# Optimization experiments

Hardware: AMD Instinct MI355X
Metric: run time of the kernel (lower is better)

The kernel has to match this reference:

```python
import jax, jax.numpy as jnp
import numpy as np

NUM_CLASSES = 512  # P distinct identities in the batch (labels are in [0, P))
TAU = 0.5
EPS = 1e-12


def _l2norm(x):
    # F.normalize(x, dim=1) with eps clamp
    n = jnp.sqrt(jnp.sum(x * x, axis=1, keepdims=True))
    return x / jnp.maximum(n, EPS)


def setup_inputs() -> dict:
    key = jax.random.key(0)
    k1, k2, k3 = jax.random.split(key, 3)
    N, D, P = 8192, 2048, NUM_CLASSES
    feat_vp = jax.random.normal(k1, (N, D), dtype=jnp.float32)
    feat_ap = jax.random.normal(k2, (N, D), dtype=jnp.float32)
    feat_rp = jax.random.normal(k3, (N, D), dtype=jnp.float32)
    # P identities, K = N/P instances each; every class present
    label = (jnp.arange(N) % P).astype(jnp.int32)
    return {"feat_vp": feat_vp, "feat_ap": feat_ap, "feat_rp": feat_rp, "label": label}


def reference(feat_vp, feat_ap, feat_rp, label):
    P = NUM_CLASSES
    fv = _l2norm(feat_vp)
    fa = _l2norm(feat_ap)
    fr = _l2norm(feat_rp)

    # segment-mean over labels (replaces the O(N^2 D) python loop)
    counts = jax.ops.segment_sum(jnp.ones_like(label, dtype=fv.dtype), label,
                                 num_segments=P)  # [P]
    inv_cnt = 1.0 / counts[:, None]

    def centers(f):
        s = jax.ops.segment_sum(f, label, num_segments=P)  # [P, D]
        return _l2norm(s * inv_cnt)

    cv, ca, cr = centers(fv), centers(fa), centers(fr)

    # per-sample centers = unique centers gathered back by label
    loss_intra = (jnp.sum((fv - cv[label]) ** 2, axis=1).mean()
                  + jnp.sum((fa - ca[label]) ** 2, axis=1).mean()
                  + jnp.sum((fr - cr[label]) ** 2, axis=1).mean())

    def pair_loss(c1, c2):
        logits = (c1 @ c2.T) / TAU  # [P, P]
        logp = jax.nn.log_softmax(logits, axis=1)
        return -jnp.mean(jnp.diagonal(logp))

    loss_inter = pair_loss(cv, ca) + pair_loss(cv, cr) + pair_loss(ca, cr)
    return loss_intra + loss_inter
```

## Files before the change

### kernel.cpp

```cpp
#include <hip/hip_runtime.h>
#include <hip/hip_bf16.h>

#define P_CLS 512
#define D_DIM 2048
#define CAP   32
#define TAU_INV 2.0f

typedef short short8 __attribute__((ext_vector_type(8)));
typedef float f32x4 __attribute__((ext_vector_type(4)));

__device__ __forceinline__ unsigned short f2bf_bits(float x) {
  __hip_bfloat16 b = __float2bfloat16(x);
  unsigned short u;
  __builtin_memcpy(&u, &b, sizeof(u));
  return u;
}

__device__ __forceinline__ float xred_sum(float v) {
#pragma unroll
  for (int o = 1; o < 64; o <<= 1) v += __shfl_xor(v, o, 64);
  return v;
}
__device__ __forceinline__ float xred_max(float v) {
#pragma unroll
  for (int o = 1; o < 64; o <<= 1) v = fmaxf(v, __shfl_xor(v, o, 64));
  return v;
}

__global__ void k_init(int* cnt, float* accs) {
  int t = blockIdx.x * blockDim.x + threadIdx.x;
  if (t < P_CLS) cnt[t] = 0;
  if (t < 8) accs[t] = 0.f;
}

__global__ void k_index(const int* __restrict__ label, int* __restrict__ cnt,
                        int* __restrict__ idx, int n) {
  int i = blockIdx.x * blockDim.x + threadIdx.x;
  if (i < n) {
    int p = label[i];
    int slot = atomicAdd(&cnt[p], 1);
    if (slot < CAP) idx[p * CAP + slot] = i;
  }
}

__global__ __launch_bounds__(256)
void k_centers(const float* __restrict__ f0, const float* __restrict__ f1,
               const float* __restrict__ f2, const int* __restrict__ cnt,
               const int* __restrict__ idx, __hip_bfloat16* __restrict__ cb,
               float* __restrict__ accs) {
  __shared__ __align__(16) f32x4 red[4][D_DIM / 4];
  __shared__ float scr[4];
  int p = blockIdx.x, m = blockIdx.y;
  const float* F = (m == 0) ? f0 : (m == 1) ? f1 : f2;
  int t = threadIdx.x, lane = t & 63, wv = t >> 6;
  int c = cnt[p];
  if (c > CAP) c = CAP;
  const int* idxp = idx + p * CAP;

  int nr = (c > wv) ? ((c - wv + 3) >> 2) : 0;

  const f32x4* rp[8];
#pragma unroll
  for (int k = 0; k < 8; ++k) {
    int r = wv + 4 * k;
    int rc = (r < c) ? r : 0;
    rp[k] = (c > 0) ? (const f32x4*)(F + (long)idxp[rc] * D_DIM) + lane
                    : (const f32x4*)F + lane;
  }

  f32x4 acc[8] = {{0,0,0,0},{0,0,0,0},{0,0,0,0},{0,0,0,0},
                  {0,0,0,0},{0,0,0,0},{0,0,0,0},{0,0,0,0}};
  f32x4 ba[8], bb[8], bd[8];

  auto loadrow = [&](f32x4* buf, const f32x4* src) {
#pragma unroll
    for (int j = 0; j < 8; ++j) buf[j] = src[64 * j];
    asm volatile("" : "+v"(buf[0]), "+v"(buf[1]), "+v"(buf[2]), "+v"(buf[3]),
                      "+v"(buf[4]), "+v"(buf[5]), "+v"(buf[6]), "+v"(buf[7]));
  };
  auto consume = [&](const f32x4* buf) {
    float ssq = 0.f;
#pragma unroll
    for (int j = 0; j < 8; ++j) {
      f32x4 q = buf[j] * buf[j];
      ssq += q.x + q.y + q.z + q.w;
    }
    ssq = xred_sum(ssq);
    float w = 1.0f / fmaxf(sqrtf(ssq), 1e-12f);
#pragma unroll
    for (int j = 0; j < 8; ++j) acc[j] += buf[j] * w;
  };

  if (nr > 0) loadrow(ba, rp[0]);
  if (nr > 1) loadrow(bb, rp[1]);
  if (nr > 2) loadrow(bd, rp[2]);
#pragma unroll
  for (int k = 0; k < 8; ++k) {
    f32x4* cur = (k % 3 == 0) ? ba : (k % 3 == 1) ? bb : bd;
    if (k < nr) consume(cur);
    if (k + 3 < nr) loadrow(cur, rp[k + 3]);
  }

#pragma unroll
  for (int j = 0; j < 8; ++j) red[wv][lane + 64 * j] = acc[j];
  __syncthreads();
  f32x4 s0 = red[0][t] + red[1][t] + red[2][t] + red[3][t];
  f32x4 s1 = red[0][t + 256] + red[1][t + 256] + red[2][t + 256] + red[3][t + 256];
  f32x4 q0 = s0 * s0, q1 = s1 * s1;
  float s2 = q0.x + q0.y + q0.z + q0.w + q1.x + q1.y + q1.z + q1.w;
  s2 = xred_sum(s2);
  if (lane == 0) scr[wv] = s2;
  __syncthreads();
  s2 = scr[0] + scr[1] + scr[2] + scr[3];
  float sn = sqrtf(s2);
  float inv = 1.0f / fmaxf(sn, 1e-12f);
  __hip_bfloat16* dst = cb + ((long)m * P_CLS + p) * D_DIM;
  f32x4 o0 = s0 * inv, o1 = s1 * inv;
  ushort4 h0, h1;
  h0.x = f2bf_bits(o0.x); h0.y = f2bf_bits(o0.y);
  h0.z = f2bf_bits(o0.z); h0.w = f2bf_bits(o0.w);
  h1.x = f2bf_bits(o1.x); h1.y = f2bf_bits(o1.y);
  h1.z = f2bf_bits(o1.z); h1.w = f2bf_bits(o1.w);
  ((ushort4*)dst)[t] = h0;
  ((ushort4*)dst)[t + 256] = h1;
  if (t == 0 && c > 0) atomicAdd(&accs[0], sn);
}

__global__ __launch_bounds__(256)
void k_gemm(const __hip_bfloat16* __restrict__ cbh, float* __restrict__ logits) {
  __shared__ __align__(16) unsigned short As[2][128 * 40], Bs[2][128 * 40];
  int pair = blockIdx.y, kz = blockIdx.z, nkz = gridDim.z;
  int ksl = D_DIM / nkz;
  int ma = (pair == 2) ? 1 : 0;
  int mb = (pair == 0) ? 1 : 2;
  const unsigned short* A =
      (const unsigned short*)cbh + (long)ma * P_CLS * D_DIM + kz * ksl;
  const unsigned short* B =
      (const unsigned short*)cbh + (long)mb * P_CLS * D_DIM + kz * ksl;
  float* C = logits + ((long)kz * 3 + pair) * P_CLS * P_CLS;
  int tm = (blockIdx.x & 3) * 128, tn = (blockIdx.x >> 2) * 128;
  int t = threadIdx.x, lane = t & 63, wv = t >> 6;
  int quad = lane >> 4, mr = lane & 15;
  int wr = (wv >> 1) * 64, wc = (wv & 1) * 64;
  int sr0 = t >> 2, sc0 = (t & 3) * 8;
  int sr1 = (t + 256) >> 2, sc1 = ((t + 256) & 3) * 8;
  const unsigned short* pa0 = A + (long)(tm + sr0) * D_DIM + sc0;
  const unsigned short* pa1 = A + (long)(tm + sr1) * D_DIM + sc1;
  const unsigned short* pb0 = B + (long)(tn + sr0) * D_DIM + sc0;
  const unsigned short* pb1 = B + (long)(tn + sr1) * D_DIM + sc1;
  int l0 = sr0 * 40 + sc0, l1 = sr1 * 40 + sc1;

  f32x4 acc[4][4];
#pragma unroll
  for (int i = 0; i < 4; ++i)
#pragma unroll
    for (int j = 0; j < 4; ++j) acc[i][j] = {0, 0, 0, 0};

  uint4 a0 = *(const uint4*)pa0, a1 = *(const uint4*)pa1;
  uint4 b0 = *(const uint4*)pb0, b1 = *(const uint4*)pb1;
  *(uint4*)(&As[0][l0]) = a0; *(uint4*)(&As[0][l1]) = a1;
  *(uint4*)(&Bs[0][l0]) = b0; *(uint4*)(&Bs[0][l1]) = b1;
  a0 = *(const uint4*)(pa0 + 32); a1 = *(const uint4*)(pa1 + 32);
  b0 = *(const uint4*)(pb0 + 32); b1 = *(const uint4*)(pb1 + 32);

  const int NIT = ksl / 32;
  for (int it = 0; it < NIT; ++it) {
    __syncthreads();
    int cur = it & 1;
    if (it + 1 < NIT) {
      *(uint4*)(&As[cur ^ 1][l0]) = a0; *(uint4*)(&As[cur ^ 1][l1]) = a1;
      *(uint4*)(&Bs[cur ^ 1][l0]) = b0; *(uint4*)(&Bs[cur ^ 1][l1]) = b1;
    }
    if (it + 2 < NIT) {
      a0 = *(const uint4*)(pa0 + (it + 2) * 32);
      a1 = *(const uint4*)(pa1 + (it + 2) * 32);
      b0 = *(const uint4*)(pb0 + (it + 2) * 32);
      b1 = *(const uint4*)(pb1 + (it + 2) * 32);
    }
    short8 af[4], bf[4];
#pragma unroll
    for (int i = 0; i < 4; ++i)
      af[i] = *(const short8*)(&As[cur][(wr + i * 16 + mr) * 40 + quad * 8]);
#pragma unroll
    for (int j = 0; j < 4; ++j)
      bf[j] = *(const short8*)(&Bs[cur][(wc + j * 16 + mr) * 40 + quad * 8]);
#pragma unroll
    for (int i = 0; i < 4; ++i)
#pragma unroll
      for (int j = 0; j < 4; ++j)
        acc[i][j] = __builtin_amdgcn_mfma_f32_16x16x32_bf16(af[i], bf[j],
                                                            acc[i][j], 0, 0, 0);
  }
#pragma unroll
  for (int i = 0; i < 4; ++i) {
    int crow = tm + wr + i * 16 + quad * 4;
#pragma unroll
    for (int j = 0; j < 4; ++j) {
      int ccol = tn + wc + j * 16 + mr;
#pragma unroll
      for (int r = 0; r < 4; ++r)
        C[(long)(crow + r) * P_CLS + ccol] = acc[i][j][r] * TAU_INV;
    }
  }
}

__global__ __launch_bounds__(256)
void k_lse(const float* __restrict__ logits, float* __restrict__ lsep, int nkz) {
  __shared__ float sred[12];
  int row = blockIdx.x;
  int p = row & (P_CLS - 1);
  int t = threadIdx.x, lane = t & 63, wv = t >> 6;
  float v0 = 0.f, v1 = 0.f;
  for (int z = 0; z < nkz; ++z) {
    const float* L = logits + ((long)z * 3 * P_CLS + row) * P_CLS;
    v0 += L[t];
    v1 += L[t + 256];
  }
  float dg = 0.f;
  if (t == p) dg = v0;
  if (t + 256 == p) dg = v1;
  float mx = xred_max(fmaxf(v0, v1));
  if (lane == 0) sred[wv] = mx;
  __syncthreads();
  mx = fmaxf(fmaxf(sred[0], sred[1]), fmaxf(sred[2], sred[3]));
  float e = expf(v0 - mx) + expf(v1 - mx);
  e = xred_sum(e);
  dg = xred_sum(dg);
  if (lane == 0) { sred[4 + wv] = e; sred[8 + wv] = dg; }
  __syncthreads();
  if (t == 0) {
    float tot = sred[4] + sred[5] + sred[6] + sred[7];
    float dgt = sred[8] + sred[9] + sred[10] + sred[11];
    lsep[row] = mx + logf(tot) - dgt;
  }
}

__global__ __launch_bounds__(256)
void k_final(const float* __restrict__ accs, const float* __restrict__ lsep,
             float* __restrict__ out, float invN) {
  __shared__ float sr[4];
  int t = threadIdx.x, lane = t & 63, wv = t >> 6;
  float s = 0.f;
#pragma unroll
  for (int i = 0; i < 6; ++i) s += lsep[t + 256 * i];
  s = xred_sum(s);
  if (lane == 0) sr[wv] = s;
  __syncthreads();
  if (t == 0) {
    float tot = sr[0] + sr[1] + sr[2] + sr[3];
    out[0] = 6.0f - 2.0f * invN * accs[0] + tot * (1.0f / (float)P_CLS);
  }
}

extern "C" void kernel_launch(void* const* d_in, const int* in_sizes, int n_in,
                              void* d_out, int out_size, void* d_ws, size_t ws_size,
                              hipStream_t stream) {
  const float* fvp = (const float*)d_in[0];
  const float* fap = (const float*)d_in[1];
  const float* frp = (const float*)d_in[2];
  const int* label = (const int*)d_in[3];
  int N = in_sizes[3];

  char* ws = (char*)d_ws;
  int* cnt = (int*)ws;
  int* idx = (int*)(ws + 2048);
  float* accs = (float*)(ws + 2048 + 65536);
  float* lsep = (float*)(ws + 69632);
  __hip_bfloat16* cb = (__hip_bfloat16*)(ws + 131072);
  float* logits = (float*)(ws + 131072 + 3ul * P_CLS * D_DIM * 2);

  size_t base = 131072 + 3ul * P_CLS * D_DIM * 2;
  size_t per_z = 3ul * P_CLS * P_CLS * 4;
  int KZ = (ws_size >= base + 8 * per_z) ? 8
         : (ws_size >= base + 4 * per_z) ? 4 : 2;

  hipLaunchKernelGGL(k_init, dim3(1), dim3(512), 0, stream, cnt, accs);
  hipLaunchKernelGGL(k_index, dim3((N + 255) / 256), dim3(256), 0, stream,
                     label, cnt, idx, N);
  hipLaunchKernelGGL(k_centers, dim3(P_CLS, 3), dim3(256), 0, stream,
                     fvp, fap, frp, cnt, idx, cb, accs);
  hipLaunchKernelGGL(k_gemm, dim3(16, 3, KZ), dim3(256), 0, stream, cb, logits);
  hipLaunchKernelGGL(k_lse, dim3(3 * P_CLS), dim3(256), 0, stream, logits, lsep, KZ);
  hipLaunchKernelGGL(k_final, dim3(1), dim3(256), 0, stream, accs, lsep,
                     (float*)d_out, 1.0f / (float)N);
}
```

Measured before the change: 223.7 us.

## Fuse label indexing into centers kernel and drop init/index launches

Removes the init and index kernels. Each centers block now scans the full label array itself, collecting its class's row indices in shared memory with LDS atomics. Per-class norms go to a buffer reduced in the final kernel instead of a global float atomic. The split-K factor is capped at 4 instead of 8. This saves two launches and a global atomic pass, but every one of the 1536 blocks now reads all 8192 labels (redundant L2 traffic), and the order of sample indices within a class becomes nondeterministic.

```diff
diff --git a/kernel.cpp b/kernel.cpp
--- a/kernel.cpp
+++ b/kernel.cpp
@@ -27,35 +27,33 @@
   return v;
 }
 
-__global__ void k_init(int* cnt, float* accs) {
-  int t = blockIdx.x * blockDim.x + threadIdx.x;
-  if (t < P_CLS) cnt[t] = 0;
-  if (t < 8) accs[t] = 0.f;
-}
-
-__global__ void k_index(const int* __restrict__ label, int* __restrict__ cnt,
-                        int* __restrict__ idx, int n) {
-  int i = blockIdx.x * blockDim.x + threadIdx.x;
-  if (i < n) {
-    int p = label[i];
-    int slot = atomicAdd(&cnt[p], 1);
-    if (slot < CAP) idx[p * CAP + slot] = i;
-  }
-}
-
 __global__ __launch_bounds__(256)
 void k_centers(const float* __restrict__ f0, const float* __restrict__ f1,
-               const float* __restrict__ f2, const int* __restrict__ cnt,
-               const int* __restrict__ idx, __hip_bfloat16* __restrict__ cb,
-               float* __restrict__ accs) {
+               const float* __restrict__ f2, const int* __restrict__ label,
+               int n, __hip_bfloat16* __restrict__ cb,
+               float* __restrict__ snbuf) {
   __shared__ __align__(16) f32x4 red[4][D_DIM / 4];
   __shared__ float scr[4];
+  __shared__ int lidx[CAP];
+  __shared__ int lcnt;
   int p = blockIdx.x, m = blockIdx.y;
   const float* F = (m == 0) ? f0 : (m == 1) ? f1 : f2;
   int t = threadIdx.x, lane = t & 63, wv = t >> 6;
-  int c = cnt[p];
+
+  if (t == 0) lcnt = 0;
+  __syncthreads();
+  const int4* lab4 = (const int4*)label;
+  int n4 = n >> 2;
+  for (int i = t; i < n4; i += 256) {
+    int4 lv = lab4[i];
+    if (lv.x == p) { int s = atomicAdd(&lcnt, 1); if (s < CAP) lidx[s] = 4 * i; }
+    if (lv.y == p) { int s = atomicAdd(&lcnt, 1); if (s < CAP) lidx[s] = 4 * i + 1; }
+    if (lv.z == p) { int s = atomicAdd(&lcnt, 1); if (s < CAP) lidx[s] = 4 * i + 2; }
+    if (lv.w == p) { int s = atomicAdd(&lcnt, 1); if (s < CAP) lidx[s] = 4 * i + 3; }
+  }
+  __syncthreads();
+  int c = lcnt;
   if (c > CAP) c = CAP;
-  const int* idxp = idx + p * CAP;
 
   int nr = (c > wv) ? ((c - wv + 3) >> 2) : 0;
 
@@ -64,7 +62,7 @@
   for (int k = 0; k < 8; ++k) {
     int r = wv + 4 * k;
     int rc = (r < c) ? r : 0;
-    rp[k] = (c > 0) ? (const f32x4*)(F + (long)idxp[rc] * D_DIM) + lane
+    rp[k] = (c > 0) ? (const f32x4*)(F + (long)lidx[rc] * D_DIM) + lane
                     : (const f32x4*)F + lane;
   }
 
@@ -123,7 +121,7 @@
   h1.z = f2bf_bits(o1.z); h1.w = f2bf_bits(o1.w);
   ((ushort4*)dst)[t] = h0;
   ((ushort4*)dst)[t + 256] = h1;
-  if (t == 0 && c > 0) atomicAdd(&accs[0], sn);
+  if (t == 0) snbuf[m * P_CLS + p] = (c > 0) ? sn : 0.f;
 }
 
 __global__ __launch_bounds__(256)
@@ -236,19 +234,24 @@
 }
 
 __global__ __launch_bounds__(256)
-void k_final(const float* __restrict__ accs, const float* __restrict__ lsep,
+void k_final(const float* __restrict__ snbuf, const float* __restrict__ lsep,
              float* __restrict__ out, float invN) {
-  __shared__ float sr[4];
-  int t = threadIdx.x, lane = t & 63, wv = t >> 6;
-  float s = 0.f;
-#pragma unroll
-  for (int i = 0; i < 6; ++i) s += lsep[t + 256 * i];
+  __shared__ float sr[8];
+  int t = threadIdx.x, lane = t & 63, wv = t >> 6;
+  float s = 0.f, l = 0.f;
+#pragma unroll
+  for (int i = 0; i < 6; ++i) {
+    s += snbuf[t + 256 * i];
+    l += lsep[t + 256 * i];
+  }
   s = xred_sum(s);
-  if (lane == 0) sr[wv] = s;
+  l = xred_sum(l);
+  if (lane == 0) { sr[wv] = s; sr[4 + wv] = l; }
   __syncthreads();
   if (t == 0) {
-    float tot = sr[0] + sr[1] + sr[2] + sr[3];
-    out[0] = 6.0f - 2.0f * invN * accs[0] + tot * (1.0f / (float)P_CLS);
+    float sn_tot = sr[0] + sr[1] + sr[2] + sr[3];
+    float lse_tot = sr[4] + sr[5] + sr[6] + sr[7];
+    out[0] = 6.0f - 2.0f * invN * sn_tot + lse_tot * (1.0f / (float)P_CLS);
   }
 }
 
@@ -262,25 +265,19 @@
   int N = in_sizes[3];
 
   char* ws = (char*)d_ws;
-  int* cnt = (int*)ws;
-  int* idx = (int*)(ws + 2048);
-  float* accs = (float*)(ws + 2048 + 65536);
-  float* lsep = (float*)(ws + 69632);
-  __hip_bfloat16* cb = (__hip_bfloat16*)(ws + 131072);
-  float* logits = (float*)(ws + 131072 + 3ul * P_CLS * D_DIM * 2);
-
-  size_t base = 131072 + 3ul * P_CLS * D_DIM * 2;
+  float* snbuf = (float*)ws;
+  float* lsep = (float*)(ws + 8192);
+  __hip_bfloat16* cb = (__hip_bfloat16*)(ws + 65536);
+  float* logits = (float*)(ws + 65536 + 3ul * P_CLS * D_DIM * 2);
+
+  size_t base = 65536 + 3ul * P_CLS * D_DIM * 2;
   size_t per_z = 3ul * P_CLS * P_CLS * 4;
-  int KZ = (ws_size >= base + 8 * per_z) ? 8
-         : (ws_size >= base + 4 * per_z) ? 4 : 2;
-
-  hipLaunchKernelGGL(k_init, dim3(1), dim3(512), 0, stream, cnt, accs);
-  hipLaunchKernelGGL(k_index, dim3((N + 255) / 256), dim3(256), 0, stream,
-                     label, cnt, idx, N);
+  int KZ = (ws_size >= base + 4 * per_z) ? 4 : 2;
+
   hipLaunchKernelGGL(k_centers, dim3(P_CLS, 3), dim3(256), 0, stream,
-                     fvp, fap, frp, cnt, idx, cb, accs);
+                     fvp, fap, frp, label, N, cb, snbuf);
   hipLaunchKernelGGL(k_gemm, dim3(16, 3, KZ), dim3(256), 0, stream, cb, logits);
   hipLaunchKernelGGL(k_lse, dim3(3 * P_CLS), dim3(256), 0, stream, logits, lsep, KZ);
-  hipLaunchKernelGGL(k_final, dim3(1), dim3(256), 0, stream, accs, lsep,
+  hipLaunchKernelGGL(k_final, dim3(1), dim3(256), 0, stream, snbuf, lsep,
                      (float*)d_out, 1.0f / (float)N);
 }
```

New measurement: 220.7 us. About the same (-1.3%).
